# Kernel optimization log

Hardware: AMD Instinct MI355X
Metric: run time of the kernel (lower is better)

Reference implementation:

```python
import jax, jax.numpy as jnp
import numpy as np

B, S, D, H = 128, 256, 256, 8
EPS = 1e-5

def ln(x, g, b):
    m = x.mean(-1, keepdims=True)
    v = x.var(-1, keepdims=True)
    return (x - m) / jnp.sqrt(v + EPS) * g + b

def setup_inputs() -> dict:
    key = jax.random.key(0)
    ks = jax.random.split(key, 16)
    w = lambda k, sh: (jax.random.normal(k, sh, dtype=jnp.float32) * 0.02)
    HD = H * D
    return {
        "local": jax.random.normal(ks[0], (B, D), dtype=jnp.float32),
        "dist": jax.random.normal(ks[1], (B, S, D), dtype=jnp.float32),
        "sites": jax.random.normal(ks[2], (B, S, D), dtype=jnp.float32),
        "mask": jax.random.randint(ks[3], (B, 1, S), 0, 2).astype(bool),
        "Wq": w(ks[4], (D, HD)), "bq": jnp.zeros((HD,), jnp.float32),
        "gq": jnp.ones((HD,), jnp.float32), "betq": jnp.zeros((HD,), jnp.float32),
        "Wk": w(ks[5], (D, HD)), "bk": jnp.zeros((HD,), jnp.float32),
        "gk": jnp.ones((HD,), jnp.float32), "betk": jnp.zeros((HD,), jnp.float32),
        "Wv": w(ks[6], (D, HD)), "bv": jnp.zeros((HD,), jnp.float32),
        "gv": jnp.ones((HD,), jnp.float32), "betv": jnp.zeros((HD,), jnp.float32),
        "g1": jnp.ones((HD,), jnp.float32), "b1": jnp.zeros((HD,), jnp.float32),
        "Wo": w(ks[7], (HD, D)), "bo": jnp.zeros((D,), jnp.float32),
        "g2": jnp.ones((D,), jnp.float32), "b2": jnp.zeros((D,), jnp.float32),
        "Wa": w(ks[8], (H, 1)), "ba": jnp.zeros((1,), jnp.float32),
        "ga": jnp.ones((1,), jnp.float32), "beta_a": jnp.zeros((1,), jnp.float32),
    }

def reference(local, dist, sites, mask, Wq, bq, gq, betq, Wk, bk, gk, betk,
              Wv, bv, gv, betv, g1, b1, Wo, bo, g2, b2, Wa, ba, ga, beta_a):
    # QKV projections + LayerNorm over H*D
    q = ln(local @ Wq + bq, gq, betq)            # [B, H*D]
    k = ln(dist @ Wk + bk, gk, betk)             # [B, S, H*D]
    v = ln(sites @ Wv + bv, gv, betv)            # [B, S, H*D]
    # split heads, layout [H, B, q/s, D] matching torch permute(2,0,1,3)
    q4 = q.reshape(B, 1, H, D).transpose(2, 0, 1, 3)   # [H,B,1,D]
    k4 = k.reshape(B, S, H, D).transpose(2, 0, 1, 3)   # [H,B,S,D]
    v4 = v.reshape(B, S, H, D).transpose(2, 0, 1, 3)   # [H,B,S,D]
    u = jnp.einsum('hbqd,hbsd->hbqs', q4, k4) / jnp.sqrt(jnp.float32(S))
    u = jnp.where(mask[None], -jnp.inf, u)             # mask [B,1,S] broadcasts over heads
    attn = jax.nn.softmax(u, axis=-1)                  # [H,B,1,S]
    out = jnp.einsum('hbqs,hbsd->hbqd', attn, v4) + q4 # residual add, [H,B,1,D]
    out = out.transpose(1, 2, 0, 3).reshape(B, 1, H * D)
    out = ln(ln(out, g1, b1) @ Wo + bo, g2, b2)        # [B,1,D]
    # faithful raw view: [B,1,H,S] contiguous reinterpreted as [B,S,H]
    attn_r = attn.transpose(1, 2, 0, 3).reshape(B, S, H)
    a = ln(attn_r @ Wa + ba, ga, beta_a)               # [B,S,1]
    a = jnp.swapaxes(a, -1, -2)                        # [B,1,S]
    return (a, out)
```

## Files before the change

kernel.cpp:

```cpp
#include <hip/hip_runtime.h>

#define NB 128
#define NS 256
#define ND 256
#define NH 8
#define NHD 2048
static constexpr float EPS = 1e-5f;

typedef __attribute__((ext_vector_type(8))) short bf8v;
typedef __attribute__((ext_vector_type(4))) float f32x4;

__device__ __forceinline__ short f2bf(float f) {
  unsigned u = __float_as_uint(f);
  unsigned r = (u + 0x7fffu + ((u >> 16) & 1u)) >> 16;
  return (short)r;
}

__device__ __forceinline__ void split8(float4 a, float4 b, bf8v& hi, bf8v& lo) {
  float x[8] = {a.x, a.y, a.z, a.w, b.x, b.y, b.z, b.w};
  bf8v h, l;
#pragma unroll
  for (int i = 0; i < 8; ++i) {
    unsigned u = __float_as_uint(x[i]);
    unsigned hb = (u + 0x7fffu + ((u >> 16) & 1u)) >> 16;
    h[i] = (short)hb;
    float hf = __uint_as_float(hb << 16);
    l[i] = f2bf(x[i] - hf);
  }
  hi = h;
  lo = l;
}

__device__ __forceinline__ float block_reduce_sum(float v, float* red, int t) {
  __syncthreads();
  red[t] = v;
  __syncthreads();
  for (int off = 128; off > 0; off >>= 1) {
    if (t < off) red[t] += red[t + off];
    __syncthreads();
  }
  return red[0];
}

__global__ __launch_bounds__(256) void k_meta(const float* __restrict__ Wk,
                                              const float* __restrict__ bk,
                                              const float* __restrict__ Wv,
                                              const float* __restrict__ bv,
                                              float* __restrict__ kmeta,
                                              float* __restrict__ vmeta) {
  int sel = blockIdx.y, c = blockIdx.x, t = threadIdx.x;
  const float* W = sel ? Wv : Wk;
  const float* bvec = sel ? bv : bk;
  float* meta = sel ? vmeta : kmeta;
  __shared__ float red[256];
  float s_w = 0.f, s_l = 0.f;
  const float* row = W + (size_t)c * NHD;
  for (int j = t; j < NHD; j += 256) { float w = row[j]; s_w += w; s_l += w * bvec[j]; }
  s_w = block_reduce_sum(s_w, red, t);
  s_l = block_reduce_sum(s_l, red, t);
  if (t == 0) { meta[c] = s_w * (1.0f / NHD); meta[256 + c] = s_l * (2.0f / NHD); }
  if (c == 0) {
    float s_b = 0.f, s_b2 = 0.f;
    for (int j = t; j < NHD; j += 256) { float bb = bvec[j]; s_b += bb; s_b2 += bb * bb; }
    s_b = block_reduce_sum(s_b, red, t);
    s_b2 = block_reduce_sum(s_b2, red, t);
    if (t == 0) { meta[512] = s_b * (1.0f / NHD); meta[513] = s_b2 * (1.0f / NHD); }
  }
}

__global__ __launch_bounds__(256) void k_aat2(const float* __restrict__ Wk,
                                              const float* __restrict__ Wv,
                                              float* __restrict__ MkP,
                                              float* __restrict__ MvP) {
  int bi = blockIdx.x, bj = blockIdx.y;
  int sel = blockIdx.z & 1, kchunk = blockIdx.z >> 1;
  const float* A = sel ? Wv : Wk;
  float* outP = (sel ? MvP : MkP) + kchunk * 65536;
  int t = threadIdx.x;
  int w = t >> 6, l = t & 63, r16 = l & 15, ksub = l >> 4;
  __shared__ float red[4][32][33];

  int k0 = kchunk * 512 + w * 128;
  const float* ar0 = A + (size_t)(bi * 32 + r16) * NHD + k0;
  const float* ar1 = ar0 + 16 * NHD;
  const float* br0 = A + (size_t)(bj * 32 + r16) * NHD + k0;
  const float* br1 = br0 + 16 * NHD;

  bf8v ah[2][4], al[2][4], bh[2][4], bl[2][4];
#pragma unroll
  for (int kk = 0; kk < 4; ++kk) {
    int c0 = kk * 32 + ksub * 8;
    split8(*(const float4*)(ar0 + c0), *(const float4*)(ar0 + c0 + 4), ah[0][kk], al[0][kk]);
    split8(*(const float4*)(ar1 + c0), *(const float4*)(ar1 + c0 + 4), ah[1][kk], al[1][kk]);
    split8(*(const float4*)(br0 + c0), *(const float4*)(br0 + c0 + 4), bh[0][kk], bl[0][kk]);
    split8(*(const float4*)(br1 + c0), *(const float4*)(br1 + c0 + 4), bh[1][kk], bl[1][kk]);
  }
  f32x4 acc[2][2];
#pragma unroll
  for (int gi = 0; gi < 2; ++gi)
#pragma unroll
    for (int gj = 0; gj < 2; ++gj) acc[gi][gj] = (f32x4){0.f, 0.f, 0.f, 0.f};
#pragma unroll
  for (int kk = 0; kk < 4; ++kk) {
#pragma unroll
    for (int gi = 0; gi < 2; ++gi)
#pragma unroll
      for (int gj = 0; gj < 2; ++gj) {
        acc[gi][gj] = __builtin_amdgcn_mfma_f32_16x16x32_bf16(ah[gi][kk], bh[gj][kk], acc[gi][gj], 0, 0, 0);
        acc[gi][gj] = __builtin_amdgcn_mfma_f32_16x16x32_bf16(al[gi][kk], bh[gj][kk], acc[gi][gj], 0, 0, 0);
        acc[gi][gj] = __builtin_amdgcn_mfma_f32_16x16x32_bf16(ah[gi][kk], bl[gj][kk], acc[gi][gj], 0, 0, 0);
      }
  }
#pragma unroll
  for (int gi = 0; gi < 2; ++gi)
#pragma unroll
    for (int gj = 0; gj < 2; ++gj)
#pragma unroll
      for (int q = 0; q < 4; ++q)
        red[w][gi * 16 + ksub * 4 + q][gj * 16 + r16] = acc[gi][gj][q];
  __syncthreads();
  int r = t >> 3, c0 = (t & 7) * 4;
#pragma unroll
  for (int c = c0; c < c0 + 4; ++c) {
    float s = (red[0][r][c] + red[1][r][c]) + (red[2][r][c] + red[3][r][c]);
    outP[(size_t)(bi * 32 + r) * 256 + bj * 32 + c] = s;
  }
}

__global__ __launch_bounds__(256) void k_aat_reduce(const float* __restrict__ MkP,
                                                    const float* __restrict__ MvP,
                                                    short* __restrict__ Mkb,
                                                    short* __restrict__ Mvb) {
  int sel = blockIdx.y;
  const float* P = sel ? MvP : MkP;
  short* O = sel ? Mvb : Mkb;
  int idx = blockIdx.x * 256 + threadIdx.x;
  float s = (P[idx] + P[65536 + idx] + P[131072 + idx] + P[196608 + idx]) * (1.0f / NHD);
  O[idx] = f2bf(s);
}

__global__ __launch_bounds__(256) void k_q1(const float* __restrict__ local,
                                            const float* __restrict__ Wq,
                                            const float* __restrict__ bq,
                                            float* __restrict__ qraw,
                                            float* __restrict__ qpart) {
  int h = blockIdx.x, b = blockIdx.y, t = threadIdx.x;
  __shared__ float ls[256];
  __shared__ float red[256];
  ls[t] = local[b * ND + t];
  __syncthreads();
  int j = h * 256 + t;
  float a0 = 0.f, a1 = 0.f, a2 = 0.f, a3 = 0.f;
  const float* W = Wq + j;
#pragma unroll 4
  for (int c = 0; c < 256; c += 4) {
    a0 = fmaf(ls[c],     W[(size_t)c * NHD], a0);
    a1 = fmaf(ls[c + 1], W[(size_t)(c + 1) * NHD], a1);
    a2 = fmaf(ls[c + 2], W[(size_t)(c + 2) * NHD], a2);
    a3 = fmaf(ls[c + 3], W[(size_t)(c + 3) * NHD], a3);
  }
  float acc = (a0 + a1) + (a2 + a3) + bq[j];
  qraw[(size_t)b * NHD + j] = acc;
  float s1 = block_reduce_sum(acc, red, t);
  float s2 = block_reduce_sum(acc * acc, red, t);
  if (t == 0) { qpart[(b * 8 + h) * 2] = s1; qpart[(b * 8 + h) * 2 + 1] = s2; }
}

__global__ __launch_bounds__(256) void k_q2(const float* __restrict__ qraw,
                                            const float* __restrict__ qpart,
                                            const float* __restrict__ gq,
                                            const float* __restrict__ betq,
                                            float* __restrict__ q_ln) {
  int b = blockIdx.x, t = threadIdx.x;
  float s1 = 0.f, s2 = 0.f;
#pragma unroll
  for (int i = 0; i < 8; ++i) { s1 += qpart[(b * 8 + i) * 2]; s2 += qpart[(b * 8 + i) * 2 + 1]; }
  float m = s1 * (1.0f / NHD);
  float var = s2 * (1.0f / NHD) - m * m;
  float is = 1.0f / sqrtf(var + EPS);
#pragma unroll
  for (int r = 0; r < 8; ++r) {
    int j = r * 256 + t;
    float v = qraw[(size_t)b * NHD + j];
    q_ln[(size_t)b * NHD + j] = (v - m) * is * gq[j] + betq[j];
  }
}

__global__ __launch_bounds__(256) void k_wkeff(const float* __restrict__ q_ln,
                                               const float* __restrict__ Wk,
                                               const float* __restrict__ bk,
                                               const float* __restrict__ gk,
                                               const float* __restrict__ betk,
                                               float* __restrict__ wkeff,
                                               float* __restrict__ cbGT) {
  int h = blockIdx.x, b = blockIdx.y, t = threadIdx.x;
  __shared__ float qg[256];
  __shared__ float red[256];
  int j = h * 256 + t;
  float q = q_ln[(size_t)b * NHD + j];
  float qgv = q * gk[j];
  qg[t] = qgv;
  float cb = block_reduce_sum(bk[j] * qgv, red, t);
  float G = block_reduce_sum(qgv, red, t);
  float T = block_reduce_sum(q * betk[j], red, t);
  float acc = 0.f;
  const float4* wr = (const float4*)(Wk + (size_t)t * NHD + h * 256);
#pragma unroll 4
  for (int d4 = 0; d4 < 64; ++d4) {
    float4 w = wr[d4];
    acc += w.x * qg[d4 * 4] + w.y * qg[d4 * 4 + 1] + w.z * qg[d4 * 4 + 2] + w.w * qg[d4 * 4 + 3];
  }
  wkeff[(size_t)(b * NH + h) * ND + t] = acc;
  if (t == 0) { float* p = cbGT + (b * NH + h) * 4; p[0] = cb; p[1] = G; p[2] = T; }
}

__global__ __launch_bounds__(256) void k_maskflag(const int* __restrict__ mask_i,
                                                  int* __restrict__ flag) {
  __shared__ int s;
  int t = threadIdx.x;
  if (t == 0) s = 0;
  __syncthreads();
  int any = 0;
  for (int i = t; i < 8192; i += 256) {
    unsigned v = (unsigned)mask_i[i];
    if (v > 1u) any = 1;
  }
  if (any) atomicOr(&s, 1);
  __syncthreads();
  if (t == 0) flag[0] = s;
}

__global__ __launch_bounds__(256) void k_moments(const float* __restrict__ dist,
                                                 const float* __restrict__ sites,
                                                 const short* __restrict__ Mkb,
                                                 const short* __restrict__ Mvb,
                                                 const float* __restrict__ kmeta,
                                                 const float* __restrict__ vmeta,
                                                 float* __restrict__ mk_arr,
                                                 float* __restrict__ sk_arr,
                                                 float* __restrict__ mv_arr,
                                                 float* __restrict__ sv_arr) {
  int sel = blockIdx.y;
  const float* X = sel ? sites : dist;
  const short* Mb = sel ? Mvb : Mkb;
  const float* meta = sel ? vmeta : kmeta;
  float* m_out = sel ? mv_arr : mk_arr;
  float* s_out = sel ? sv_arr : sk_arr;

  int t = threadIdx.x;
  int w = t >> 6;
  int l = t & 63;
  int r16 = l & 15;
  int ksub = l >> 4;

  __shared__ __align__(16) short Tb[4][16][40];
  __shared__ __align__(16) short Ms[2][16][264];

  int srow = t >> 4, scol = (t & 15) * 16;

  {
    const short* src = Mb + ((size_t)srow << 8) + scol;
    *(bf8v*)&Ms[0][srow][scol] = *(const bf8v*)src;
    *(bf8v*)&Ms[0][srow][scol + 8] = *(const bf8v*)(src + 8);
  }

  size_t rowA = (size_t)blockIdx.x * 64 + w * 16;
  const float* xr0 = X + (rowA + r16) * 256;

  bf8v af0[8];
  float pm0 = 0.f, pl0 = 0.f;
#pragma unroll
  for (int kc = 0; kc < 8; ++kc) {
    int c0 = kc * 32 + ksub * 8;
    float4 wa = *(const float4*)(meta + c0);
    float4 wb = *(const float4*)(meta + c0 + 4);
    float4 la = *(const float4*)(meta + 256 + c0);
    float4 lb = *(const float4*)(meta + 256 + c0 + 4);
    float4 x0a = *(const float4*)(xr0 + c0);
    float4 x0b = *(const float4*)(xr0 + c0 + 4);
    pm0 += x0a.x * wa.x + x0a.y * wa.y + x0a.z * wa.z + x0a.w * wa.w
         + x0b.x * wb.x + x0b.y * wb.y + x0b.z * wb.z + x0b.w * wb.w;
    pl0 += x0a.x * la.x + x0a.y * la.y + x0a.z * la.z + x0a.w * la.w
         + x0b.x * lb.x + x0b.y * lb.y + x0b.z * lb.z + x0b.w * lb.w;
    bf8v a0;
    a0[0] = f2bf(x0a.x); a0[1] = f2bf(x0a.y); a0[2] = f2bf(x0a.z); a0[3] = f2bf(x0a.w);
    a0[4] = f2bf(x0b.x); a0[5] = f2bf(x0b.y); a0[6] = f2bf(x0b.z); a0[7] = f2bf(x0b.w);
    af0[kc] = a0;
  }
  pm0 += __shfl_xor(pm0, 16); pm0 += __shfl_xor(pm0, 32);
  pl0 += __shfl_xor(pl0, 16); pl0 += __shfl_xor(pl0, 32);

  __syncthreads();

  f32x4 y0 = {0.f, 0.f, 0.f, 0.f};

#pragma unroll
  for (int n = 0; n < 16; ++n) {
    if (n < 15) {
      const short* src = Mb + ((size_t)((n + 1) * 16 + srow) << 8) + scol;
      *(bf8v*)&Ms[(n + 1) & 1][srow][scol] = *(const bf8v*)src;
      *(bf8v*)&Ms[(n + 1) & 1][srow][scol + 8] = *(const bf8v*)(src + 8);
    }
    f32x4 ta = {0.f, 0.f, 0.f, 0.f};
#pragma unroll
    for (int kc = 0; kc < 8; ++kc) {
      bf8v bfv = *(const bf8v*)&Ms[n & 1][r16][kc * 32 + ksub * 8];
      ta = __builtin_amdgcn_mfma_f32_16x16x32_bf16(af0[kc], bfv, ta, 0, 0, 0);
    }
#pragma unroll
    for (int q = 0; q < 4; ++q)
      Tb[w][ksub * 4 + q][(n & 1) * 16 + r16] = f2bf(ta[q]);
    if (n & 1) {
      bf8v a20 = *(const bf8v*)&Tb[w][r16][ksub * 8];
      y0 = __builtin_amdgcn_mfma_f32_16x16x32_bf16(a20, af0[n >> 1], y0, 0, 0, 0);
    }
    __syncthreads();
  }

  int qs = r16 & 3;
  float yd0 = (qs == 0) ? y0[0] : (qs == 1) ? y0[1] : (qs == 2) ? y0[2] : y0[3];
  float bbar = meta[512], cc = meta[513];
  if (ksub == (r16 >> 2)) {
    float m0 = pm0 + bbar;
    float var0 = fmaxf(yd0 + (pl0 + cc) - m0 * m0, 0.0f) + EPS;
    m_out[rowA + r16] = m0;
    s_out[rowA + r16] = 1.0f / sqrtf(var0);
  }
}

__global__ __launch_bounds__(512) void k_attn2(const float* __restrict__ dist,
                                               const float* __restrict__ sites,
                                               const int* __restrict__ mask_i,
                                               const int* __restrict__ mflag,
                                               const float* __restrict__ wkeff,
                                               const float* __restrict__ cbGT,
                                               const float* __restrict__ mk_arr,
                                               const float* __restrict__ sk_arr,
                                               const float* __restrict__ mv_arr,
                                               const float* __restrict__ sv_arr,
                                               float* __restrict__ zbuf,
                                               float* __restrict__ bg) {
  int b = blockIdx.x, t = threadIdx.x;
  int w = t >> 6, l = t & 63, r16 = l & 15, ksub = l >> 4;

  __shared__ float us[16][260];
  __shared__ __align__(16) short St[256][72];

  for (int i = t; i < 8 * 260; i += 512) (&us[8][0])[i] = 0.f;

  const int mbytes = mflag[0];

  const float* xr0 = dist + ((size_t)b * NS + w * 32 + r16) * ND;
  const float* xr1 = xr0 + 16 * ND;
  const float* wkp = wkeff + ((size_t)b * NH + (r16 & 7)) * ND;
  f32x4 u0 = {0.f, 0.f, 0.f, 0.f}, u1 = {0.f, 0.f, 0.f, 0.f};
#pragma unroll 2
  for (int kc = 0; kc < 8; ++kc) {
    int c0 = kc * 32 + ksub * 8;
    float4 xa = *(const float4*)(xr0 + c0);
    float4 xb = *(const float4*)(xr0 + c0 + 4);
    float4 ya = *(const float4*)(xr1 + c0);
    float4 yb = *(const float4*)(xr1 + c0 + 4);
    float4 wa = {0.f, 0.f, 0.f, 0.f}, wb = {0.f, 0.f, 0.f, 0.f};
    if (r16 < 8) { wa = *(const float4*)(wkp + c0); wb = *(const float4*)(wkp + c0 + 4); }
    bf8v xh, xl, yh, yl, wh, wl;
    split8(xa, xb, xh, xl);
    split8(ya, yb, yh, yl);
    split8(wa, wb, wh, wl);
    u0 = __builtin_amdgcn_mfma_f32_16x16x32_bf16(xh, wh, u0, 0, 0, 0);
    u0 = __builtin_amdgcn_mfma_f32_16x16x32_bf16(xl, wh, u0, 0, 0, 0);
    u0 = __builtin_amdgcn_mfma_f32_16x16x32_bf16(xh, wl, u0, 0, 0, 0);
    u1 = __builtin_amdgcn_mfma_f32_16x16x32_bf16(yh, wh, u1, 0, 0, 0);
    u1 = __builtin_amdgcn_mfma_f32_16x16x32_bf16(yl, wh, u1, 0, 0, 0);
    u1 = __builtin_amdgcn_mfma_f32_16x16x32_bf16(yh, wl, u1, 0, 0, 0);
  }

  float cb = 0.f, G = 0.f, T = 0.f;
  if (r16 < 8) { const float* p = cbGT + (b * NH + r16) * 4; cb = p[0]; G = p[1]; T = p[2]; }
  const unsigned char* mask_b = (const unsigned char*)mask_i;
#pragma unroll
  for (int g = 0; g < 2; ++g) {
    f32x4 uu = g ? u1 : u0;
    int base = w * 32 + g * 16 + ksub * 4;
    float4 mk4 = *(const float4*)(mk_arr + b * NS + base);
    float4 sk4 = *(const float4*)(sk_arr + b * NS + base);
    int mm[4];
    if (mbytes) {
      mm[0] = mask_b[b * NS + base];     mm[1] = mask_b[b * NS + base + 1];
      mm[2] = mask_b[b * NS + base + 2]; mm[3] = mask_b[b * NS + base + 3];
    } else {
      mm[0] = mask_i[b * NS + base];     mm[1] = mask_i[b * NS + base + 1];
      mm[2] = mask_i[b * NS + base + 2]; mm[3] = mask_i[b * NS + base + 3];
    }
    const float* mkp = (const float*)&mk4;
    const float* skp = (const float*)&sk4;
#pragma unroll
    for (int q = 0; q < 4; ++q) {
      float u = ((uu[q] + cb - mkp[q] * G) * skp[q] + T) * 0.0625f;
      if (mm[q]) u = -1e30f;
      if (r16 < 8) us[r16][base + q] = u;
    }
  }
  __syncthreads();

  {
    int h = w;
    float v[4];
#pragma unroll
    for (int i = 0; i < 4; ++i) v[i] = us[h][l + 64 * i];
    float mx = fmaxf(fmaxf(v[0], v[1]), fmaxf(v[2], v[3]));
    for (int off = 32; off > 0; off >>= 1) mx = fmaxf(mx, __shfl_xor(mx, off));
    float sum = 0.f;
#pragma unroll
    for (int i = 0; i < 4; ++i) { v[i] = expf(v[i] - mx); sum += v[i]; }
    for (int off = 32; off > 0; off >>= 1) sum += __shfl_xor(sum, off);
    float inv = 1.0f / sum;
    float bp = 0.f, gp = 0.f;
#pragma unroll
    for (int i = 0; i < 4; ++i) {
      int s = l + 64 * i;
      float a = v[i] * inv;
      float sv = sv_arr[b * NS + s];
      float mv = mv_arr[b * NS + s];
      float wv = a * sv;
      us[h][s] = wv;
      bp += wv;
      gp += wv * mv;
    }
    for (int off = 32; off > 0; off >>= 1) { bp += __shfl_xor(bp, off); gp += __shfl_xor(gp, off); }
    if (l == 0) { float* p = bg + (b * NH + h) * 2; p[0] = bp; p[1] = gp; }
  }
  __syncthreads();

  f32x4 z0 = {0.f, 0.f, 0.f, 0.f}, z1 = {0.f, 0.f, 0.f, 0.f};
  int half = t >> 8, tc = t & 255;
  for (int chunk = 0; chunk < 4; ++chunk) {
    const float* Sp = sites + ((size_t)b * NS + chunk * 64) * ND + tc;
#pragma unroll
    for (int it = 0; it < 4; ++it) {
      int s8 = (half * 4 + it) * 8;
      bf8v vtmp;
#pragma unroll
      for (int j = 0; j < 8; ++j) vtmp[j] = f2bf(Sp[(size_t)(s8 + j) * ND]);
      *(bf8v*)&St[tc][s8] = vtmp;
    }
    __syncthreads();
#pragma unroll
    for (int kst = 0; kst < 2; ++kst) {
      int sg = chunk * 64 + kst * 32 + ksub * 8;
      int sl0 = kst * 32 + ksub * 8;
      float4 p0 = *(const float4*)&us[r16][sg];
      float4 p1 = *(const float4*)&us[r16][sg + 4];
      bf8v ah, al;
      split8(p0, p1, ah, al);
      bf8v b0 = *(const bf8v*)&St[(2 * w) * 16 + r16][sl0];
      bf8v b1 = *(const bf8v*)&St[(2 * w + 1) * 16 + r16][sl0];
      z0 = __builtin_amdgcn_mfma_f32_16x16x32_bf16(ah, b0, z0, 0, 0, 0);
      z0 = __builtin_amdgcn_mfma_f32_16x16x32_bf16(al, b0, z0, 0, 0, 0);
      z1 = __builtin_amdgcn_mfma_f32_16x16x32_bf16(ah, b1, z1, 0, 0, 0);
      z1 = __builtin_amdgcn_mfma_f32_16x16x32_bf16(al, b1, z1, 0, 0, 0);
    }
    __syncthreads();
  }
  if (ksub < 2) {
#pragma unroll
    for (int q = 0; q < 4; ++q) {
      int h = ksub * 4 + q;
      zbuf[((size_t)b * NH + h) * ND + 2 * w * 16 + r16] = z0[q];
      zbuf[((size_t)b * NH + h) * ND + (2 * w + 1) * 16 + r16] = z1[q];
    }
  }
}

__global__ __launch_bounds__(256) void k_o1(const float* __restrict__ zbuf,
                                            const float* __restrict__ bg,
                                            const float* __restrict__ q_ln,
                                            const float* __restrict__ Wv,
                                            const float* __restrict__ bv,
                                            const float* __restrict__ gv,
                                            const float* __restrict__ betv,
                                            float* __restrict__ o_buf,
                                            float* __restrict__ part1) {
  int h = blockIdx.x, b = blockIdx.y, t = threadIdx.x;
  __shared__ float zs[256];
  __shared__ float red[256];
  zs[t] = zbuf[((size_t)b * NH + h) * ND + t];
  __syncthreads();
  float bets = bg[(b * NH + h) * 2], gams = bg[(b * NH + h) * 2 + 1];
  int j = h * 256 + t;
  float a0 = 0.f, a1 = 0.f, a2 = 0.f, a3 = 0.f;
  const float* W = Wv + j;
#pragma unroll 4
  for (int c = 0; c < 256; c += 4) {
    a0 = fmaf(zs[c],     W[(size_t)c * NHD], a0);
    a1 = fmaf(zs[c + 1], W[(size_t)(c + 1) * NHD], a1);
    a2 = fmaf(zs[c + 2], W[(size_t)(c + 2) * NHD], a2);
    a3 = fmaf(zs[c + 3], W[(size_t)(c + 3) * NHD], a3);
  }
  float acc = (a0 + a1) + (a2 + a3);
  float o = gv[j] * (acc + bv[j] * bets - gams) + betv[j] + q_ln[(size_t)b * NHD + j];
  o_buf[(size_t)b * NHD + j] = o;
  float s1 = block_reduce_sum(o, red, t);
  float s2 = block_reduce_sum(o * o, red, t);
  if (t == 0) { part1[(b * 8 + h) * 2] = s1; part1[(b * 8 + h) * 2 + 1] = s2; }
}

__global__ __launch_bounds__(256) void k_o2(const float* __restrict__ o_buf,
                                            const float* __restrict__ part1,
                                            const float* __restrict__ g1,
                                            const float* __restrict__ b1,
                                            const float* __restrict__ Wo,
                                            float* __restrict__ part2) {
  int ks = blockIdx.x, b = blockIdx.y, t = threadIdx.x;
  __shared__ float y1s[256];
  float s1 = 0.f, s2 = 0.f;
#pragma unroll
  for (int i = 0; i < 8; ++i) { s1 += part1[(b * 8 + i) * 2]; s2 += part1[(b * 8 + i) * 2 + 1]; }
  float m = s1 * (1.0f / NHD);
  float var = s2 * (1.0f / NHD) - m * m;
  float is = 1.0f / sqrtf(var + EPS);
  int jj = ks * 256 + t;
  y1s[t] = (o_buf[(size_t)b * NHD + jj] - m) * is * g1[jj] + b1[jj];
  __syncthreads();
  float a0 = 0.f, a1 = 0.f, a2 = 0.f, a3 = 0.f;
  const float* W = Wo + (size_t)ks * 256 * 256 + t;
#pragma unroll 4
  for (int i = 0; i < 256; i += 4) {
    a0 = fmaf(y1s[i],     W[(size_t)i * 256], a0);
    a1 = fmaf(y1s[i + 1], W[(size_t)(i + 1) * 256], a1);
    a2 = fmaf(y1s[i + 2], W[(size_t)(i + 2) * 256], a2);
    a3 = fmaf(y1s[i + 3], W[(size_t)(i + 3) * 256], a3);
  }
  part2[((size_t)ks * NB + b) * 256 + t] = (a0 + a1) + (a2 + a3);
}

__global__ __launch_bounds__(256) void k_o3(const float* __restrict__ part2,
                                            const float* __restrict__ bo,
                                            const float* __restrict__ g2,
                                            const float* __restrict__ b2,
                                            const float* __restrict__ beta_a,
                                            float* __restrict__ out) {
  int b = blockIdx.x, t = threadIdx.x;
  __shared__ float red[256];
  float acc = bo[t];
#pragma unroll
  for (int ks = 0; ks < 8; ++ks) acc += part2[((size_t)ks * NB + b) * 256 + t];
  float q1 = block_reduce_sum(acc, red, t);
  float q2 = block_reduce_sum(acc * acc, red, t);
  float m2 = q1 * (1.0f / 256.0f);
  float v2 = q2 * (1.0f / 256.0f) - m2 * m2;
  float is2 = 1.0f / sqrtf(v2 + EPS);
  out[NB * NS + b * 256 + t] = (acc - m2) * is2 * g2[t] + b2[t];
  out[b * 256 + t] = beta_a[0];
}

extern "C" void kernel_launch(void* const* d_in, const int* in_sizes, int n_in,
                              void* d_out, int out_size, void* d_ws, size_t ws_size,
                              hipStream_t stream) {
  (void)in_sizes; (void)n_in; (void)out_size; (void)ws_size;
  const float* local = (const float*)d_in[0];
  const float* dist  = (const float*)d_in[1];
  const float* sites = (const float*)d_in[2];
  const int*   mask  = (const int*)d_in[3];
  const float* Wq   = (const float*)d_in[4];
  const float* bq   = (const float*)d_in[5];
  const float* gq   = (const float*)d_in[6];
  const float* betq = (const float*)d_in[7];
  const float* Wk   = (const float*)d_in[8];
  const float* bk   = (const float*)d_in[9];
  const float* gk   = (const float*)d_in[10];
  const float* betk = (const float*)d_in[11];
  const float* Wv   = (const float*)d_in[12];
  const float* bv   = (const float*)d_in[13];
  const float* gv   = (const float*)d_in[14];
  const float* betv = (const float*)d_in[15];
  const float* g1   = (const float*)d_in[16];
  const float* b1   = (const float*)d_in[17];
  const float* Wo   = (const float*)d_in[18];
  const float* bo   = (const float*)d_in[19];
  const float* g2   = (const float*)d_in[20];
  const float* b2   = (const float*)d_in[21];
  const float* beta_a = (const float*)d_in[25];
  float* out = (float*)d_out;

  float* ws = (float*)d_ws;
  float* MkP   = ws;
  float* MvP   = MkP + 262144;
  short* Mkb   = (short*)(MvP + 262144);
  short* Mvb   = Mkb + 65536;
  float* kmeta = (float*)(Mvb + 65536);
  float* vmeta = kmeta + 1024;
  float* q_ln  = vmeta + 1024;
  float* wkeff = q_ln + 262144;
  float* cbGT  = wkeff + 262144;
  float* mk_arr = cbGT + 4096;
  float* sk_arr = mk_arr + 32768;
  float* mv_arr = sk_arr + 32768;
  float* sv_arr = mv_arr + 32768;
  float* zbuf  = sv_arr + 32768;
  float* bg    = zbuf + 262144;
  int*   mflag = (int*)(bg + 2048);
  float* part1 = (float*)(mflag + 16);
  float* qpart = part1 + 2048;

  float* qraw  = MkP;
  float* o_buf = MkP;
  float* part2 = MvP;

  k_meta<<<dim3(256, 2), dim3(256), 0, stream>>>(Wk, bk, Wv, bv, kmeta, vmeta);
  k_aat2<<<dim3(8, 8, 8), dim3(256), 0, stream>>>(Wk, Wv, MkP, MvP);
  k_aat_reduce<<<dim3(256, 2), dim3(256), 0, stream>>>(MkP, MvP, Mkb, Mvb);
  k_q1<<<dim3(8, 128), dim3(256), 0, stream>>>(local, Wq, bq, qraw, qpart);
  k_q2<<<dim3(128), dim3(256), 0, stream>>>(qraw, qpart, gq, betq, q_ln);
  k_wkeff<<<dim3(8, 128), dim3(256), 0, stream>>>(q_ln, Wk, bk, gk, betk, wkeff, cbGT);
  k_maskflag<<<dim3(1), dim3(256), 0, stream>>>(mask, mflag);
  k_moments<<<dim3(512, 2), dim3(256), 0, stream>>>(dist, sites, Mkb, Mvb, kmeta, vmeta,
                                                    mk_arr, sk_arr, mv_arr, sv_arr);
  k_attn2<<<dim3(128), dim3(512), 0, stream>>>(dist, sites, mask, mflag, wkeff, cbGT,
                                               mk_arr, sk_arr, mv_arr, sv_arr, zbuf, bg);
  k_o1<<<dim3(8, 128), dim3(256), 0, stream>>>(zbuf, bg, q_ln, Wv, bv, gv, betv, o_buf, part1);
  k_o2<<<dim3(8, 128), dim3(256), 0, stream>>>(o_buf, part1, g1, b1, Wo, part2);
  k_o3<<<dim3(128), dim3(256), 0, stream>>>(part2, bo, g2, b2, beta_a, out);
}
```

Measured before the change: 160.3 us.

## Fuse mask flag and q LayerNorm into neighbours, exploit Gram symmetry, drop LDS staging

The mask-validity scan now runs inside k_meta, and the q LayerNorm kernel is removed: k_wkeff and k_o1 each recompute the normalisation from qraw and the partial sums. This drops two launches and one intermediate buffer. k_aat2 exploits the symmetry of W·Wᵀ by computing only the upper-triangle 32x32 tiles and writing the transposed tile as well, which cuts the MFMA work to 36 of 64 tiles. k_moments replaces its double-buffered LDS staging of the bf16 matrix, and the barriers that went with it, with direct global loads per wave. The cost is redundant LN recomputation and more global-memory traffic on the B operand in k_moments.

```diff
diff --git a/kernel.cpp b/kernel.cpp
--- a/kernel.cpp
+++ b/kernel.cpp
@@ -46,13 +46,16 @@
                                               const float* __restrict__ bk,
                                               const float* __restrict__ Wv,
                                               const float* __restrict__ bv,
+                                              const int* __restrict__ mask_i,
                                               float* __restrict__ kmeta,
-                                              float* __restrict__ vmeta) {
+                                              float* __restrict__ vmeta,
+                                              int* __restrict__ flag) {
   int sel = blockIdx.y, c = blockIdx.x, t = threadIdx.x;
   const float* W = sel ? Wv : Wk;
   const float* bvec = sel ? bv : bk;
   float* meta = sel ? vmeta : kmeta;
   __shared__ float red[256];
+  __shared__ int sflag;
   float s_w = 0.f, s_l = 0.f;
   const float* row = W + (size_t)c * NHD;
   for (int j = t; j < NHD; j += 256) { float w = row[j]; s_w += w; s_l += w * bvec[j]; }
@@ -66,14 +69,28 @@
     s_b2 = block_reduce_sum(s_b2, red, t);
     if (t == 0) { meta[512] = s_b * (1.0f / NHD); meta[513] = s_b2 * (1.0f / NHD); }
   }
+  if (c == 1 && sel == 0) {
+    if (t == 0) sflag = 0;
+    __syncthreads();
+    int any = 0;
+    for (int i = t; i < 8192; i += 256) {
+      unsigned v = (unsigned)mask_i[i];
+      if (v > 1u) any = 1;
+    }
+    if (any) atomicOr(&sflag, 1);
+    __syncthreads();
+    if (t == 0) flag[0] = sflag;
+  }
 }
 
 __global__ __launch_bounds__(256) void k_aat2(const float* __restrict__ Wk,
                                               const float* __restrict__ Wv,
                                               float* __restrict__ MkP,
                                               float* __restrict__ MvP) {
-  int bi = blockIdx.x, bj = blockIdx.y;
-  int sel = blockIdx.z & 1, kchunk = blockIdx.z >> 1;
+  int idx = blockIdx.x, bi = 0;
+  while (idx >= 8 - bi) { idx -= 8 - bi; ++bi; }
+  int bj = bi + idx;
+  int sel = blockIdx.y & 1, kchunk = blockIdx.y >> 1;
   const float* A = sel ? Wv : Wk;
   float* outP = (sel ? MvP : MkP) + kchunk * 65536;
   int t = threadIdx.x;
@@ -124,6 +141,13 @@
   for (int c = c0; c < c0 + 4; ++c) {
     float s = (red[0][r][c] + red[1][r][c]) + (red[2][r][c] + red[3][r][c]);
     outP[(size_t)(bi * 32 + r) * 256 + bj * 32 + c] = s;
+  }
+  if (bi != bj) {
+#pragma unroll
+    for (int c = c0; c < c0 + 4; ++c) {
+      float s = (red[0][c][r] + red[1][c][r]) + (red[2][c][r] + red[3][c][r]);
+      outP[(size_t)(bj * 32 + r) * 256 + bi * 32 + c] = s;
+    }
   }
 }
 
@@ -166,27 +190,10 @@
   if (t == 0) { qpart[(b * 8 + h) * 2] = s1; qpart[(b * 8 + h) * 2 + 1] = s2; }
 }
 
-__global__ __launch_bounds__(256) void k_q2(const float* __restrict__ qraw,
-                                            const float* __restrict__ qpart,
-                                            const float* __restrict__ gq,
-                                            const float* __restrict__ betq,
-                                            float* __restrict__ q_ln) {
-  int b = blockIdx.x, t = threadIdx.x;
-  float s1 = 0.f, s2 = 0.f;
-#pragma unroll
-  for (int i = 0; i < 8; ++i) { s1 += qpart[(b * 8 + i) * 2]; s2 += qpart[(b * 8 + i) * 2 + 1]; }
-  float m = s1 * (1.0f / NHD);
-  float var = s2 * (1.0f / NHD) - m * m;
-  float is = 1.0f / sqrtf(var + EPS);
-#pragma unroll
-  for (int r = 0; r < 8; ++r) {
-    int j = r * 256 + t;
-    float v = qraw[(size_t)b * NHD + j];
-    q_ln[(size_t)b * NHD + j] = (v - m) * is * gq[j] + betq[j];
-  }
-}
-
-__global__ __launch_bounds__(256) void k_wkeff(const float* __restrict__ q_ln,
+__global__ __launch_bounds__(256) void k_wkeff(const float* __restrict__ qraw,
+                                               const float* __restrict__ qpart,
+                                               const float* __restrict__ gq,
+                                               const float* __restrict__ betq,
                                                const float* __restrict__ Wk,
                                                const float* __restrict__ bk,
                                                const float* __restrict__ gk,
@@ -196,8 +203,14 @@
   int h = blockIdx.x, b = blockIdx.y, t = threadIdx.x;
   __shared__ float qg[256];
   __shared__ float red[256];
+  float s1 = 0.f, s2 = 0.f;
+#pragma unroll
+  for (int i = 0; i < 8; ++i) { s1 += qpart[(b * 8 + i) * 2]; s2 += qpart[(b * 8 + i) * 2 + 1]; }
+  float m = s1 * (1.0f / NHD);
+  float var = s2 * (1.0f / NHD) - m * m;
+  float is = 1.0f / sqrtf(var + EPS);
   int j = h * 256 + t;
-  float q = q_ln[(size_t)b * NHD + j];
+  float q = (qraw[(size_t)b * NHD + j] - m) * is * gq[j] + betq[j];
   float qgv = q * gk[j];
   qg[t] = qgv;
   float cb = block_reduce_sum(bk[j] * qgv, red, t);
@@ -212,22 +225,6 @@
   }
   wkeff[(size_t)(b * NH + h) * ND + t] = acc;
   if (t == 0) { float* p = cbGT + (b * NH + h) * 4; p[0] = cb; p[1] = G; p[2] = T; }
-}
-
-__global__ __launch_bounds__(256) void k_maskflag(const int* __restrict__ mask_i,
-                                                  int* __restrict__ flag) {
-  __shared__ int s;
-  int t = threadIdx.x;
-  if (t == 0) s = 0;
-  __syncthreads();
-  int any = 0;
-  for (int i = t; i < 8192; i += 256) {
-    unsigned v = (unsigned)mask_i[i];
-    if (v > 1u) any = 1;
-  }
-  if (any) atomicOr(&s, 1);
-  __syncthreads();
-  if (t == 0) flag[0] = s;
 }
 
 __global__ __launch_bounds__(256) void k_moments(const float* __restrict__ dist,
@@ -254,15 +251,6 @@
   int ksub = l >> 4;
 
   __shared__ __align__(16) short Tb[4][16][40];
-  __shared__ __align__(16) short Ms[2][16][264];
-
-  int srow = t >> 4, scol = (t & 15) * 16;
-
-  {
-    const short* src = Mb + ((size_t)srow << 8) + scol;
-    *(bf8v*)&Ms[0][srow][scol] = *(const bf8v*)src;
-    *(bf8v*)&Ms[0][srow][scol + 8] = *(const bf8v*)(src + 8);
-  }
 
   size_t rowA = (size_t)blockIdx.x * 64 + w * 16;
   const float* xr0 = X + (rowA + r16) * 256;
@@ -290,23 +278,18 @@
   pm0 += __shfl_xor(pm0, 16); pm0 += __shfl_xor(pm0, 32);
   pl0 += __shfl_xor(pl0, 16); pl0 += __shfl_xor(pl0, 32);
 
-  __syncthreads();
-
   f32x4 y0 = {0.f, 0.f, 0.f, 0.f};
 
 #pragma unroll
   for (int n = 0; n < 16; ++n) {
-    if (n < 15) {
-      const short* src = Mb + ((size_t)((n + 1) * 16 + srow) << 8) + scol;
-      *(bf8v*)&Ms[(n + 1) & 1][srow][scol] = *(const bf8v*)src;
-      *(bf8v*)&Ms[(n + 1) & 1][srow][scol + 8] = *(const bf8v*)(src + 8);
-    }
+    bf8v bf[8];
+#pragma unroll
+    for (int kc = 0; kc < 8; ++kc)
+      bf[kc] = *(const bf8v*)(Mb + ((size_t)(n * 16 + r16) << 8) + kc * 32 + ksub * 8);
     f32x4 ta = {0.f, 0.f, 0.f, 0.f};
 #pragma unroll
-    for (int kc = 0; kc < 8; ++kc) {
-      bf8v bfv = *(const bf8v*)&Ms[n & 1][r16][kc * 32 + ksub * 8];
-      ta = __builtin_amdgcn_mfma_f32_16x16x32_bf16(af0[kc], bfv, ta, 0, 0, 0);
-    }
+    for (int kc = 0; kc < 8; ++kc)
+      ta = __builtin_amdgcn_mfma_f32_16x16x32_bf16(af0[kc], bf[kc], ta, 0, 0, 0);
 #pragma unroll
     for (int q = 0; q < 4; ++q)
       Tb[w][ksub * 4 + q][(n & 1) * 16 + r16] = f2bf(ta[q]);
@@ -314,7 +297,6 @@
       bf8v a20 = *(const bf8v*)&Tb[w][r16][ksub * 8];
       y0 = __builtin_amdgcn_mfma_f32_16x16x32_bf16(a20, af0[n >> 1], y0, 0, 0, 0);
     }
-    __syncthreads();
   }
 
   int qs = r16 & 3;
@@ -474,7 +456,10 @@
 
 __global__ __launch_bounds__(256) void k_o1(const float* __restrict__ zbuf,
                                             const float* __restrict__ bg,
-                                            const float* __restrict__ q_ln,
+                                            const float* __restrict__ qraw,
+                                            const float* __restrict__ qpart,
+                                            const float* __restrict__ gq,
+                                            const float* __restrict__ betq,
                                             const float* __restrict__ Wv,
                                             const float* __restrict__ bv,
                                             const float* __restrict__ gv,
@@ -486,6 +471,12 @@
   __shared__ float red[256];
   zs[t] = zbuf[((size_t)b * NH + h) * ND + t];
   __syncthreads();
+  float qs1 = 0.f, qs2 = 0.f;
+#pragma unroll
+  for (int i = 0; i < 8; ++i) { qs1 += qpart[(b * 8 + i) * 2]; qs2 += qpart[(b * 8 + i) * 2 + 1]; }
+  float qm = qs1 * (1.0f / NHD);
+  float qvar = qs2 * (1.0f / NHD) - qm * qm;
+  float qis = 1.0f / sqrtf(qvar + EPS);
   float bets = bg[(b * NH + h) * 2], gams = bg[(b * NH + h) * 2 + 1];
   int j = h * 256 + t;
   float a0 = 0.f, a1 = 0.f, a2 = 0.f, a3 = 0.f;
@@ -498,7 +489,8 @@
     a3 = fmaf(zs[c + 3], W[(size_t)(c + 3) * NHD], a3);
   }
   float acc = (a0 + a1) + (a2 + a3);
-  float o = gv[j] * (acc + bv[j] * bets - gams) + betv[j] + q_ln[(size_t)b * NHD + j];
+  float qln = (qraw[(size_t)b * NHD + j] - qm) * qis * gq[j] + betq[j];
+  float o = gv[j] * (acc + bv[j] * bets - gams) + betv[j] + qln;
   o_buf[(size_t)b * NHD + j] = o;
   float s1 = block_reduce_sum(o, red, t);
   float s2 = block_reduce_sum(o * o, red, t);
@@ -590,8 +582,8 @@
   short* Mvb   = Mkb + 65536;
   float* kmeta = (float*)(Mvb + 65536);
   float* vmeta = kmeta + 1024;
-  float* q_ln  = vmeta + 1024;
-  float* wkeff = q_ln + 262144;
+  float* qraw  = vmeta + 1024;
+  float* wkeff = qraw + 262144;
   float* cbGT  = wkeff + 262144;
   float* mk_arr = cbGT + 4096;
   float* sk_arr = mk_arr + 32768;
@@ -603,22 +595,21 @@
   float* part1 = (float*)(mflag + 16);
   float* qpart = part1 + 2048;
 
-  float* qraw  = MkP;
-  float* o_buf = MkP;
+  float* o_buf = qraw;
   float* part2 = MvP;
 
-  k_meta<<<dim3(256, 2), dim3(256), 0, stream>>>(Wk, bk, Wv, bv, kmeta, vmeta);
-  k_aat2<<<dim3(8, 8, 8), dim3(256), 0, stream>>>(Wk, Wv, MkP, MvP);
+  k_meta<<<dim3(256, 2), dim3(256), 0, stream>>>(Wk, bk, Wv, bv, mask, kmeta, vmeta, mflag);
+  k_aat2<<<dim3(36, 8), dim3(256), 0, stream>>>(Wk, Wv, MkP, MvP);
   k_aat_reduce<<<dim3(256, 2), dim3(256), 0, stream>>>(MkP, MvP, Mkb, Mvb);
   k_q1<<<dim3(8, 128), dim3(256), 0, stream>>>(local, Wq, bq, qraw, qpart);
-  k_q2<<<dim3(128), dim3(256), 0, stream>>>(qraw, qpart, gq, betq, q_ln);
-  k_wkeff<<<dim3(8, 128), dim3(256), 0, stream>>>(q_ln, Wk, bk, gk, betk, wkeff, cbGT);
-  k_maskflag<<<dim3(1), dim3(256), 0, stream>>>(mask, mflag);
+  k_wkeff<<<dim3(8, 128), dim3(256), 0, stream>>>(qraw, qpart, gq, betq, Wk, bk, gk, betk,
+                                                  wkeff, cbGT);
   k_moments<<<dim3(512, 2), dim3(256), 0, stream>>>(dist, sites, Mkb, Mvb, kmeta, vmeta,
                                                     mk_arr, sk_arr, mv_arr, sv_arr);
   k_attn2<<<dim3(128), dim3(512), 0, stream>>>(dist, sites, mask, mflag, wkeff, cbGT,
                                                mk_arr, sk_arr, mv_arr, sv_arr, zbuf, bg);
-  k_o1<<<dim3(8, 128), dim3(256), 0, stream>>>(zbuf, bg, q_ln, Wv, bv, gv, betv, o_buf, part1);
+  k_o1<<<dim3(8, 128), dim3(256), 0, stream>>>(zbuf, bg, qraw, qpart, gq, betq,
+                                               Wv, bv, gv, betv, o_buf, part1);
   k_o2<<<dim3(8, 128), dim3(256), 0, stream>>>(o_buf, part1, g1, b1, Wo, part2);
   k_o3<<<dim3(128), dim3(256), 0, stream>>>(part2, bo, g2, b2, beta_a, out);
 }
```

Result: slower. 184.0 us (+14.8%).
